# Performance work log

Measured on AMD Instinct MI355X. Metric: run time of the kernel, lower is better.

## Reference

```python
import jax, jax.numpy as jnp
import numpy as np

K, MU, SIGMA = 8, 0.0, 0.1
M, N, D_DIM, T = 512, 1024, 512, 4096


def setup_inputs() -> dict:
    key = jax.random.key(0)
    ks, ke, ka, kd, kl1, kl2 = jax.random.split(key, 6)
    S = jax.random.normal(ks, (N, T), dtype=jnp.float32)
    E = jax.random.normal(ke, (M, T), dtype=jnp.float32)  # raw noise; scaled by sigma/mu in reference
    A = jax.random.uniform(ka, (M, N), dtype=jnp.float32)  # torch.rand init
    Dm = jax.random.normal(kd, (N, D_DIM), dtype=jnp.float32) / jnp.sqrt(N)  # stands in for DCT-transformed randn
    c = jnp.ones((1,), dtype=jnp.float32)
    l1 = 0.1 * jnp.abs(jax.random.normal(kl1, (1,), dtype=jnp.float32)) + 0.05
    l2 = jax.random.normal(kl2, (1,), dtype=jnp.float32)
    # LISTA params per layer; all K layers get the same closed-form init in the original
    U1 = jnp.eye(D_DIM, dtype=jnp.float32) - (1.0 / c[0]) * (Dm.T @ A.T @ A @ Dm)  # [d,d]
    V1 = (1.0 / c[0]) * (Dm.T @ A.T)  # [d,m]
    U = jnp.broadcast_to(U1, (K, D_DIM, D_DIM)).copy()
    V = jnp.broadcast_to(V1, (K, D_DIM, M)).copy()
    H0 = jnp.zeros((D_DIM, T), dtype=jnp.float32)
    return {"S": S, "E": E, "A": A, "D": Dm, "U": U, "V": V, "l1": l1, "l2": l2, "c": c, "H0": H0}


def reference(S, E, A, D, U, V, l1, l2, c, H0):
    # X = A @ S + noise (E ~ randn, scaled as in torch forward)
    X = A @ S + (E * SIGMA + MU)  # [m,T]
    # Self-attention on H0 (the original loop always feeds self.H, the zero buffer,
    # into every layer -- H is never chained). Attention map = softmax((D@H0)^T (D@H0)).
    G = D @ H0                                   # [n,T]
    attn = jax.nn.softmax(G.T @ G, axis=-1)      # [T,T]
    Z = l2[0] * (H0 @ attn)                      # [d,T]
    # All K LISTA updates share the same (H0-derived) Z and X -> batch over layers.
    mat = jnp.einsum('kde,et->kdt', U, Z) + jnp.einsum('kdm,mt->kdt', V, X)  # [K,d,T]
    thres = l1[0] / c[0]
    H_all = jnp.sign(mat) * jnp.maximum(jnp.zeros((), mat.dtype), jnp.abs(mat) - thres)
    H_last = H_all[-1]                           # only the last layer's H survives the loop
    return D @ H_last                            # S_star [n,T]
```

## Files before the change

kernel.cpp:

```cpp
#include <hip/hip_runtime.h>

typedef unsigned short ushort_t;
typedef unsigned int u32;
typedef ushort_t u16x8 __attribute__((ext_vector_type(8)));
typedef ushort_t u16x4 __attribute__((ext_vector_type(4)));
typedef __bf16   bf16x8 __attribute__((ext_vector_type(8)));
typedef float    f32x4  __attribute__((ext_vector_type(4)));

#define T_DIM 4096

__device__ __forceinline__ ushort_t f2bf(float f){
  union { float f; unsigned u; } x; x.f = f;
  unsigned r = x.u + 0x7FFFu + ((x.u >> 16) & 1u);
  return (ushort_t)(r >> 16);
}

__device__ __forceinline__ void gload16(const void* g, void* l){
  __builtin_amdgcn_global_load_lds(
      (const __attribute__((address_space(1))) u32*)g,
      (__attribute__((address_space(3))) u32*)l, 16, 0, 0);
}

__global__ __launch_bounds__(256) void prep_kernel(
    const float* __restrict__ S, const float* __restrict__ A,
    const float* __restrict__ V7, const float* __restrict__ Dm,
    ushort_t* __restrict__ St, ushort_t* __restrict__ Abf,
    ushort_t* __restrict__ Vbf, ushort_t* __restrict__ Dbf)
{
  __shared__ float tile[64][65];
  const int bid = blockIdx.x, tid = threadIdx.x;
  if (bid < 1024){
    const int t0 = (bid & 63) * 64, n0 = (bid >> 6) * 64;
#pragma unroll
    for (int i = 0; i < 4; ++i){
      int g = tid + 256 * i; int row = g >> 4, cq = g & 15;
      const f32x4 v = *(const f32x4*)&S[(size_t)(n0 + row) * T_DIM + t0 + cq * 4];
#pragma unroll
      for (int j = 0; j < 4; ++j) tile[row][cq * 4 + j] = v[j];
    }
    __syncthreads();
#pragma unroll
    for (int i = 0; i < 2; ++i){
      int g = tid + 256 * i; int tl = g >> 3, nq = g & 7;
      u16x8 h;
#pragma unroll
      for (int j = 0; j < 8; ++j) h[j] = f2bf(tile[nq * 8 + j][tl]);
      *(u16x8*)&St[(size_t)(t0 + tl) * 1024 + n0 + ((nq ^ (tl & 7)) << 3)] = h;
    }
  } else {
    int pid = bid - 1024;
    const float* src; ushort_t* dst; int g, ks;
    if (pid < 256)      { src = A;  dst = Abf; g = pid * 256 + tid;        ks = 7; }
    else if (pid < 384) { src = V7; dst = Vbf; g = (pid - 256) * 256 + tid; ks = 6; }
    else                { src = Dm; dst = Dbf; g = (pid - 384) * 256 + tid; ks = 6; }
    const int r = g >> ks, cg = g & ((1 << ks) - 1);
    const int Kd = 8 << ks;
    const size_t base = (size_t)r * Kd + (size_t)cg * 8;
    const f32x4 v0 = *(const f32x4*)&src[base];
    const f32x4 v1 = *(const f32x4*)&src[base + 4];
    u16x8 h;
#pragma unroll
    for (int j = 0; j < 4; ++j){ h[j] = f2bf(v0[j]); h[j + 4] = f2bf(v1[j]); }
    *(u16x8*)&dst[(size_t)r * Kd + ((cg >> 3) << 6) + ((((cg & 7) ^ (r & 7))) << 3)] = h;
  }
}

template<int EPI, int NK>
__global__ __launch_bounds__(512, 2) void gemm_kernel(
    const ushort_t* __restrict__ Ag, const ushort_t* __restrict__ Bg,
    void* __restrict__ Cout, const float* __restrict__ Eptr,
    const float* __restrict__ l1p, const float* __restrict__ cp)
{
  constexpr int KD = NK * 64;
  constexpr bool SWAP = (EPI != 2);
  constexpr int P = SWAP ? 2 : 4;
  constexpr int Q = SWAP ? 4 : 2;
  __shared__ __align__(16) ushort_t As[4][128 * 64];
  __shared__ __align__(16) ushort_t Bs[4][64 * 64];
  __shared__ __align__(16) float Elds[64 * 128];
  const int tid = threadIdx.x;
  const int lane = tid & 63, wid = tid >> 6;
  const int g = wid >> 2;
  const int s = wid & 3;
  const int wm = s >> 1, wn = s & 1;
  const int lr = lane & 15, lq = lane >> 4;
  const int t0 = blockIdx.x * 128, n0 = blockIdx.y * 64;
  const int ltid = tid & 255;

  f32x4 acc[P][Q];
#pragma unroll
  for (int p = 0; p < P; ++p)
#pragma unroll
    for (int q = 0; q < Q; ++q) acc[p][q] = (f32x4){0.f, 0.f, 0.f, 0.f};

  auto stage = [&](int kt){
    const int slot = ((kt & 1) << 1) | ((kt >> 1) & 1);
#pragma unroll
    for (int i = 0; i < 4; ++i){
      int c = i * 256 + ltid;
      gload16(&Ag[(size_t)(t0 + (c >> 3)) * KD + kt * 64 + (c & 7) * 8],
              &As[slot][(i * 256 + (ltid & 192)) * 8]);
    }
#pragma unroll
    for (int i = 0; i < 2; ++i){
      int c = i * 256 + ltid;
      gload16(&Bg[(size_t)(n0 + (c >> 3)) * KD + kt * 64 + (c & 7) * 8],
              &Bs[slot][(i * 256 + (ltid & 192)) * 8]);
    }
  };

  auto compute = [&](int kt){
    const int slot = ((kt & 1) << 1) | ((kt >> 1) & 1);
#pragma unroll
    for (int ksv = 0; ksv < 2; ++ksv){
      const int kb = ksv * 4 + lq;
      bf16x8 a[4], bb[2];
#pragma unroll
      for (int mf = 0; mf < 4; ++mf){
        int r = wm * 64 + mf * 16 + lr;
        a[mf] = *(const bf16x8*)&As[slot][r * 64 + ((kb ^ (r & 7)) << 3)];
      }
#pragma unroll
      for (int nf = 0; nf < 2; ++nf){
        int r = wn * 32 + nf * 16 + lr;
        bb[nf] = *(const bf16x8*)&Bs[slot][r * 64 + ((kb ^ (r & 7)) << 3)];
      }
      __builtin_amdgcn_s_setprio(1);
      if constexpr (SWAP){
#pragma unroll
        for (int nf = 0; nf < 2; ++nf)
#pragma unroll
          for (int mf = 0; mf < 4; ++mf)
            acc[nf][mf] = __builtin_amdgcn_mfma_f32_16x16x32_bf16(
                bb[nf], a[mf], acc[nf][mf], 0, 0, 0);
      } else {
#pragma unroll
        for (int mf = 0; mf < 4; ++mf)
#pragma unroll
          for (int nf = 0; nf < 2; ++nf)
            acc[mf][nf] = __builtin_amdgcn_mfma_f32_16x16x32_bf16(
                a[mf], bb[nf], acc[mf][nf], 0, 0, 0);
      }
      __builtin_amdgcn_s_setprio(0);
    }
  };

  if constexpr (EPI == 0){
#pragma unroll
    for (int i = 0; i < 4; ++i){
      int c = i * 512 + tid;
      gload16(&Eptr[(size_t)(n0 + (c >> 5)) * T_DIM + t0 + (c & 31) * 4],
              (char*)Elds + (size_t)(i * 512 + (tid & 448)) * 16);
    }
    __builtin_amdgcn_sched_barrier(0);
  }
  if (g == 0){ stage(0); stage(2); }
  else       { stage(1); }

  for (int kt = 0; kt < NK; ++kt){
    if ((kt & 1) == g){
      if (kt + 2 < NK) { asm volatile("s_waitcnt vmcnt(6)" ::: "memory"); }
      else             { asm volatile("s_waitcnt vmcnt(0)" ::: "memory"); }
    }
    __builtin_amdgcn_s_barrier();
    __builtin_amdgcn_sched_barrier(0);
    if ((kt & 1) == g){
      compute(kt);
    } else {
      if (kt + 3 < NK) stage(kt + 3);
    }
  }

  float* accs = (float*)&As[0][0];

  if constexpr (SWAP){
    if (g == 1){
#pragma unroll
      for (int nf = 0; nf < 2; ++nf)
#pragma unroll
        for (int mf = 0; mf < 4; ++mf){
          const int tl = wm * 64 + mf * 16 + lr;
          const int em0 = wn * 32 + nf * 16 + lq * 4;
          const int mp = (((em0 >> 3) ^ (tl & 7)) << 3) + (em0 & 7);
          *(f32x4*)&accs[tl * 68 + mp] = acc[nf][mf];
        }
    }
    asm volatile("s_waitcnt lgkmcnt(0)" ::: "memory");
    __builtin_amdgcn_s_barrier();
    if (g == 0){
      const float thres = (EPI == 1) ? (l1p[0] / cp[0]) : 0.f;
#pragma unroll
      for (int nf = 0; nf < 2; ++nf)
#pragma unroll
        for (int mf = 0; mf < 4; ++mf){
          const int tl = wm * 64 + mf * 16 + lr;
          const int em0 = wn * 32 + nf * 16 + lq * 4;
          const int mp = (((em0 >> 3) ^ (tl & 7)) << 3) + (em0 & 7);
          f32x4 v = *(const f32x4*)&accs[tl * 68 + mp];
          v += acc[nf][mf];
          if constexpr (EPI == 0){
#pragma unroll
            for (int j = 0; j < 4; ++j)
              v[j] += 0.1f * Elds[(em0 + j) * 128 + tl];
          } else {
#pragma unroll
            for (int j = 0; j < 4; ++j){
              float av = fabsf(v[j]) - thres;
              v[j] = av > 0.f ? (v[j] > 0.f ? av : -av) : 0.f;
            }
          }
          *(f32x4*)&accs[tl * 68 + mp] = v;
        }
    }
    asm volatile("s_waitcnt lgkmcnt(0)" ::: "memory");
    __builtin_amdgcn_s_barrier();
    ushort_t* OT = (ushort_t*)Cout;
#pragma unroll
    for (int i = 0; i < 2; ++i){
      const int c = i * 512 + tid;
      const int t = c >> 3, mb = (c & 7) * 8;
      const f32x4 a0 = *(const f32x4*)&accs[t * 68 + mb];
      const f32x4 a1 = *(const f32x4*)&accs[t * 68 + mb + 4];
      u16x8 h;
#pragma unroll
      for (int j = 0; j < 4; ++j){ h[j] = f2bf(a0[j]); h[j + 4] = f2bf(a1[j]); }
      *(u16x8*)&OT[(size_t)(t0 + t) * 512 + n0 + mb] = h;
    }
  } else {
    if (g == 1){
#pragma unroll
      for (int mf = 0; mf < 4; ++mf)
#pragma unroll
        for (int nf = 0; nf < 2; ++nf){
          const int tl0 = wm * 64 + mf * 16 + lq * 4;
          const int nl  = wn * 32 + nf * 16 + lr;
          *(f32x4*)&accs[nl * 132 + tl0] = acc[mf][nf];
        }
    }
    asm volatile("s_waitcnt lgkmcnt(0)" ::: "memory");
    __builtin_amdgcn_s_barrier();
    if (g == 0){
#pragma unroll
      for (int mf = 0; mf < 4; ++mf)
#pragma unroll
        for (int nf = 0; nf < 2; ++nf){
          const int tl0 = wm * 64 + mf * 16 + lq * 4;
          const int nl  = wn * 32 + nf * 16 + lr;
          f32x4 v = *(const f32x4*)&accs[nl * 132 + tl0];
          v += acc[mf][nf];
          *(f32x4*)&accs[nl * 132 + tl0] = v;
        }
    }
    asm volatile("s_waitcnt lgkmcnt(0)" ::: "memory");
    __builtin_amdgcn_s_barrier();
    float* O = (float*)Cout;
#pragma unroll
    for (int i = 0; i < 4; ++i){
      const int c = i * 512 + tid;
      const int n = c >> 5, t4 = (c & 31) * 4;
      *(f32x4*)&O[(size_t)(n0 + n) * T_DIM + t0 + t4] =
          *(const f32x4*)&accs[n * 132 + t4];
    }
  }
}

extern "C" void kernel_launch(void* const* d_in, const int* in_sizes, int n_in,
                              void* d_out, int out_size, void* d_ws, size_t ws_size,
                              hipStream_t stream)
{
  const float* S  = (const float*)d_in[0];
  const float* E  = (const float*)d_in[1];
  const float* A  = (const float*)d_in[2];
  const float* Dm = (const float*)d_in[3];
  const float* V  = (const float*)d_in[5];
  const float* l1 = (const float*)d_in[6];
  const float* c  = (const float*)d_in[8];

  char* ws = (char*)d_ws;
  ushort_t* St  = (ushort_t*)(ws);
  ushort_t* XT  = (ushort_t*)(ws + (size_t)( 8u << 20));
  ushort_t* HT  = (ushort_t*)(ws + (size_t)(12u << 20));
  ushort_t* Abf = (ushort_t*)(ws + (size_t)(16u << 20));
  ushort_t* Vbf = (ushort_t*)(ws + (size_t)(17u << 20));
  ushort_t* Dbf = (ushort_t*)(ws + (size_t)(17u << 20) + (512u << 10));
  const float* V7 = V + (size_t)7 * 512 * 512;

  prep_kernel<<<1664, 256, 0, stream>>>(S, A, V7, Dm, St, Abf, Vbf, Dbf);
  gemm_kernel<0, 16><<<dim3(32, 8), 512, 0, stream>>>(St, Abf, (void*)XT, E, nullptr, nullptr);
  gemm_kernel<1, 8><<<dim3(32, 8), 512, 0, stream>>>(XT, Vbf, (void*)HT, nullptr, l1, c);
  gemm_kernel<2, 8><<<dim3(32, 16), 512, 0, stream>>>(HT, Dbf, d_out, nullptr, nullptr, nullptr);
}
```

Measured before the change: 39.66 us.

## Fuse S transpose and bf16 conversion into first GEMM's load pipeline

Removes the separate S transpose/convert pass from the prep kernel. The first GEMM now loads fp32 S tiles into registers, converts them to bf16 and writes them transposed into LDS inside its double-buffered pipeline. This eliminates writing and re-reading the 8 MB bf16 St intermediate and shrinks the prep kernel. In exchange, each n-block re-reads S in fp32, which doubles the re-read bytes, and the extra staging registers add pressure.

```diff
diff --git a/kernel.cpp b/kernel.cpp
--- a/kernel.cpp
+++ b/kernel.cpp
@@ -22,54 +22,206 @@
 }
 
 __global__ __launch_bounds__(256) void prep_kernel(
-    const float* __restrict__ S, const float* __restrict__ A,
-    const float* __restrict__ V7, const float* __restrict__ Dm,
-    ushort_t* __restrict__ St, ushort_t* __restrict__ Abf,
+    const float* __restrict__ A, const float* __restrict__ V7,
+    const float* __restrict__ Dm, ushort_t* __restrict__ Abf,
     ushort_t* __restrict__ Vbf, ushort_t* __restrict__ Dbf)
 {
-  __shared__ float tile[64][65];
-  const int bid = blockIdx.x, tid = threadIdx.x;
-  if (bid < 1024){
-    const int t0 = (bid & 63) * 64, n0 = (bid >> 6) * 64;
-#pragma unroll
-    for (int i = 0; i < 4; ++i){
-      int g = tid + 256 * i; int row = g >> 4, cq = g & 15;
-      const f32x4 v = *(const f32x4*)&S[(size_t)(n0 + row) * T_DIM + t0 + cq * 4];
-#pragma unroll
-      for (int j = 0; j < 4; ++j) tile[row][cq * 4 + j] = v[j];
-    }
-    __syncthreads();
+  const int pid = blockIdx.x, tid = threadIdx.x;
+  const float* src; ushort_t* dst; int g, ks;
+  if (pid < 256)      { src = A;  dst = Abf; g = pid * 256 + tid;        ks = 7; }
+  else if (pid < 384) { src = V7; dst = Vbf; g = (pid - 256) * 256 + tid; ks = 6; }
+  else                { src = Dm; dst = Dbf; g = (pid - 384) * 256 + tid; ks = 6; }
+  const int r = g >> ks, cg = g & ((1 << ks) - 1);
+  const int Kd = 8 << ks;
+  const size_t base = (size_t)r * Kd + (size_t)cg * 8;
+  const f32x4 v0 = *(const f32x4*)&src[base];
+  const f32x4 v1 = *(const f32x4*)&src[base + 4];
+  u16x8 h;
+#pragma unroll
+  for (int j = 0; j < 4; ++j){ h[j] = f2bf(v0[j]); h[j + 4] = f2bf(v1[j]); }
+  *(u16x8*)&dst[(size_t)r * Kd + ((cg >> 3) << 6) + ((((cg & 7) ^ (r & 7))) << 3)] = h;
+}
+
+#define ISSUE_S(kt, rS) do {                                                   \
+  _Pragma("unroll") for (int i_ = 0; i_ < 2; ++i_){                            \
+    const int task_ = i_ * 256 + ltid;                                         \
+    const int rg_ = task_ >> 5, tq_ = task_ & 31;                              \
+    _Pragma("unroll") for (int ii_ = 0; ii_ < 4; ++ii_)                        \
+      rS[i_ * 4 + ii_] = *(const f32x4*)&S[                                    \
+          (size_t)((kt) * 64 + rg_ * 4 + ii_) * T_DIM + t0 + tq_ * 4];         \
+  } } while (0)
+
+#define WRITE_S(kt, rS) do {                                                   \
+  const int slot_ = (((kt) & 1) << 1) | (((kt) >> 1) & 1);                     \
+  _Pragma("unroll") for (int i_ = 0; i_ < 2; ++i_){                            \
+    const int task_ = i_ * 256 + ltid;                                         \
+    const int rg_ = task_ >> 5, tq_ = task_ & 31;                              \
+    _Pragma("unroll") for (int j_ = 0; j_ < 4; ++j_){                          \
+      const int t_ = tq_ * 4 + j_;                                             \
+      u16x4 w_;                                                                \
+      _Pragma("unroll") for (int ii_ = 0; ii_ < 4; ++ii_)                      \
+        w_[ii_] = f2bf(rS[i_ * 4 + ii_][j_]);                                  \
+      *(u16x4*)&As[slot_][t_ * 64 + (((rg_ >> 1) ^ (t_ & 7)) << 3)             \
+                          + ((rg_ & 1) << 2)] = w_;                            \
+    }                                                                          \
+  } } while (0)
+
+#define G1_STEP(kt, RLD, RWR) do {                                             \
+  if (((kt) & 1) == g){                                                        \
+    __builtin_amdgcn_s_barrier();                                              \
+    __builtin_amdgcn_sched_barrier(0);                                         \
+    compute(kt);                                                               \
+  } else {                                                                     \
+    if ((kt) + 3 < NK) ISSUE_S((kt) + 3, RLD);                                 \
+    __builtin_amdgcn_s_barrier();                                              \
+    if ((kt) + 3 < NK){                                                        \
+      issueB((kt) + 3);                                                        \
+      asm volatile("s_waitcnt vmcnt(10)" ::: "memory");                        \
+    } else {                                                                   \
+      asm volatile("s_waitcnt vmcnt(0)" ::: "memory");                         \
+    }                                                                          \
+    __builtin_amdgcn_sched_barrier(0);                                         \
+    if ((kt) + 1 < NK) WRITE_S((kt) + 1, RWR);                                 \
+    asm volatile("s_waitcnt lgkmcnt(0)" ::: "memory");                         \
+  } } while (0)
+
+__global__ __launch_bounds__(512, 2) void gemm1_kernel(
+    const float* __restrict__ S, const ushort_t* __restrict__ Bg,
+    const float* __restrict__ Eptr, ushort_t* __restrict__ XT)
+{
+  constexpr int NK = 16;
+  __shared__ __align__(16) ushort_t As[4][128 * 64];
+  __shared__ __align__(16) ushort_t Bs[4][64 * 64];
+  __shared__ __align__(16) float Elds[64 * 128];
+  const int tid = threadIdx.x;
+  const int lane = tid & 63, wid = tid >> 6;
+  const int g = wid >> 2, s = wid & 3;
+  const int wm = s >> 1, wn = s & 1;
+  const int lr = lane & 15, lq = lane >> 4;
+  const int t0 = blockIdx.x * 128, n0 = blockIdx.y * 64;
+  const int ltid = tid & 255;
+
+  f32x4 acc[2][4];
+#pragma unroll
+  for (int p = 0; p < 2; ++p)
+#pragma unroll
+    for (int q = 0; q < 4; ++q) acc[p][q] = (f32x4){0.f, 0.f, 0.f, 0.f};
+
+  f32x4 rSa[8], rSb[8];
+
+  auto issueB = [&](int kt){
+    const int slot = ((kt & 1) << 1) | ((kt >> 1) & 1);
 #pragma unroll
     for (int i = 0; i < 2; ++i){
-      int g = tid + 256 * i; int tl = g >> 3, nq = g & 7;
-      u16x8 h;
-#pragma unroll
-      for (int j = 0; j < 8; ++j) h[j] = f2bf(tile[nq * 8 + j][tl]);
-      *(u16x8*)&St[(size_t)(t0 + tl) * 1024 + n0 + ((nq ^ (tl & 7)) << 3)] = h;
-    }
+      int c = i * 256 + ltid;
+      gload16(&Bg[(size_t)(n0 + (c >> 3)) * 1024 + kt * 64 + (c & 7) * 8],
+              &Bs[slot][(i * 256 + (ltid & 192)) * 8]);
+    }
+  };
+
+  auto compute = [&](int kt){
+    const int slot = ((kt & 1) << 1) | ((kt >> 1) & 1);
+#pragma unroll
+    for (int ksv = 0; ksv < 2; ++ksv){
+      const int kb = ksv * 4 + lq;
+      bf16x8 a[4], bb[2];
+#pragma unroll
+      for (int mf = 0; mf < 4; ++mf){
+        int r = wm * 64 + mf * 16 + lr;
+        a[mf] = *(const bf16x8*)&As[slot][r * 64 + ((kb ^ (r & 7)) << 3)];
+      }
+#pragma unroll
+      for (int nf = 0; nf < 2; ++nf){
+        int r = wn * 32 + nf * 16 + lr;
+        bb[nf] = *(const bf16x8*)&Bs[slot][r * 64 + ((kb ^ (r & 7)) << 3)];
+      }
+      __builtin_amdgcn_s_setprio(1);
+#pragma unroll
+      for (int nf = 0; nf < 2; ++nf)
+#pragma unroll
+        for (int mf = 0; mf < 4; ++mf)
+          acc[nf][mf] = __builtin_amdgcn_mfma_f32_16x16x32_bf16(
+              bb[nf], a[mf], acc[nf][mf], 0, 0, 0);
+      __builtin_amdgcn_s_setprio(0);
+    }
+  };
+
+#pragma unroll
+  for (int i = 0; i < 4; ++i){
+    int c = i * 512 + tid;
+    gload16(&Eptr[(size_t)(n0 + (c >> 5)) * T_DIM + t0 + (c & 31) * 4],
+            (char*)Elds + (size_t)(i * 512 + (tid & 448)) * 16);
+  }
+  __builtin_amdgcn_sched_barrier(0);
+  if (g == 0){
+    ISSUE_S(0, rSa); issueB(0);
+    asm volatile("s_waitcnt vmcnt(0)" ::: "memory");
+    WRITE_S(0, rSa);
+    ISSUE_S(2, rSb); issueB(2);
   } else {
-    int pid = bid - 1024;
-    const float* src; ushort_t* dst; int g, ks;
-    if (pid < 256)      { src = A;  dst = Abf; g = pid * 256 + tid;        ks = 7; }
-    else if (pid < 384) { src = V7; dst = Vbf; g = (pid - 256) * 256 + tid; ks = 6; }
-    else                { src = Dm; dst = Dbf; g = (pid - 384) * 256 + tid; ks = 6; }
-    const int r = g >> ks, cg = g & ((1 << ks) - 1);
-    const int Kd = 8 << ks;
-    const size_t base = (size_t)r * Kd + (size_t)cg * 8;
-    const f32x4 v0 = *(const f32x4*)&src[base];
-    const f32x4 v1 = *(const f32x4*)&src[base + 4];
+    ISSUE_S(1, rSb); issueB(1);
+  }
+  asm volatile("s_waitcnt lgkmcnt(0)" ::: "memory");
+
+#pragma unroll 1
+  for (int kt0 = 0; kt0 < NK; kt0 += 4){
+    G1_STEP(kt0 + 0, rSa, rSb);
+    G1_STEP(kt0 + 1, rSa, rSb);
+    G1_STEP(kt0 + 2, rSb, rSa);
+    G1_STEP(kt0 + 3, rSb, rSa);
+  }
+  asm volatile("s_waitcnt vmcnt(0)" ::: "memory");
+
+  float* accs = (float*)&As[0][0];
+  if (g == 1){
+#pragma unroll
+    for (int nf = 0; nf < 2; ++nf)
+#pragma unroll
+      for (int mf = 0; mf < 4; ++mf){
+        const int tl = wm * 64 + mf * 16 + lr;
+        const int em0 = wn * 32 + nf * 16 + lq * 4;
+        const int mp = (((em0 >> 3) ^ (tl & 7)) << 3) + (em0 & 7);
+        *(f32x4*)&accs[tl * 68 + mp] = acc[nf][mf];
+      }
+  }
+  asm volatile("s_waitcnt lgkmcnt(0)" ::: "memory");
+  __builtin_amdgcn_s_barrier();
+  if (g == 0){
+#pragma unroll
+    for (int nf = 0; nf < 2; ++nf)
+#pragma unroll
+      for (int mf = 0; mf < 4; ++mf){
+        const int tl = wm * 64 + mf * 16 + lr;
+        const int em0 = wn * 32 + nf * 16 + lq * 4;
+        const int mp = (((em0 >> 3) ^ (tl & 7)) << 3) + (em0 & 7);
+        f32x4 v = *(const f32x4*)&accs[tl * 68 + mp];
+        v += acc[nf][mf];
+#pragma unroll
+        for (int j = 0; j < 4; ++j)
+          v[j] += 0.1f * Elds[(em0 + j) * 128 + tl];
+        *(f32x4*)&accs[tl * 68 + mp] = v;
+      }
+  }
+  asm volatile("s_waitcnt lgkmcnt(0)" ::: "memory");
+  __builtin_amdgcn_s_barrier();
+#pragma unroll
+  for (int i = 0; i < 2; ++i){
+    const int c = i * 512 + tid;
+    const int t = c >> 3, mb = (c & 7) * 8;
+    const f32x4 a0 = *(const f32x4*)&accs[t * 68 + mb];
+    const f32x4 a1 = *(const f32x4*)&accs[t * 68 + mb + 4];
     u16x8 h;
 #pragma unroll
-    for (int j = 0; j < 4; ++j){ h[j] = f2bf(v0[j]); h[j + 4] = f2bf(v1[j]); }
-    *(u16x8*)&dst[(size_t)r * Kd + ((cg >> 3) << 6) + ((((cg & 7) ^ (r & 7))) << 3)] = h;
+    for (int j = 0; j < 4; ++j){ h[j] = f2bf(a0[j]); h[j + 4] = f2bf(a1[j]); }
+    *(u16x8*)&XT[(size_t)(t0 + t) * 512 + n0 + mb] = h;
   }
 }
 
 template<int EPI, int NK>
 __global__ __launch_bounds__(512, 2) void gemm_kernel(
     const ushort_t* __restrict__ Ag, const ushort_t* __restrict__ Bg,
-    void* __restrict__ Cout, const float* __restrict__ Eptr,
-    const float* __restrict__ l1p, const float* __restrict__ cp)
+    void* __restrict__ Cout, const float* __restrict__ l1p,
+    const float* __restrict__ cp)
 {
   constexpr int KD = NK * 64;
   constexpr bool SWAP = (EPI != 2);
@@ -77,7 +229,6 @@
   constexpr int Q = SWAP ? 4 : 2;
   __shared__ __align__(16) ushort_t As[4][128 * 64];
   __shared__ __align__(16) ushort_t Bs[4][64 * 64];
-  __shared__ __align__(16) float Elds[64 * 128];
   const int tid = threadIdx.x;
   const int lane = tid & 63, wid = tid >> 6;
   const int g = wid >> 2;
@@ -145,15 +296,6 @@
     }
   };
 
-  if constexpr (EPI == 0){
-#pragma unroll
-    for (int i = 0; i < 4; ++i){
-      int c = i * 512 + tid;
-      gload16(&Eptr[(size_t)(n0 + (c >> 5)) * T_DIM + t0 + (c & 31) * 4],
-              (char*)Elds + (size_t)(i * 512 + (tid & 448)) * 16);
-    }
-    __builtin_amdgcn_sched_barrier(0);
-  }
   if (g == 0){ stage(0); stage(2); }
   else       { stage(1); }
 
@@ -172,7 +314,6 @@
   }
 
   float* accs = (float*)&As[0][0];
-
   if constexpr (SWAP){
     if (g == 1){
 #pragma unroll
@@ -188,7 +329,7 @@
     asm volatile("s_waitcnt lgkmcnt(0)" ::: "memory");
     __builtin_amdgcn_s_barrier();
     if (g == 0){
-      const float thres = (EPI == 1) ? (l1p[0] / cp[0]) : 0.f;
+      const float thres = l1p[0] / cp[0];
 #pragma unroll
       for (int nf = 0; nf < 2; ++nf)
 #pragma unroll
@@ -198,16 +339,10 @@
           const int mp = (((em0 >> 3) ^ (tl & 7)) << 3) + (em0 & 7);
           f32x4 v = *(const f32x4*)&accs[tl * 68 + mp];
           v += acc[nf][mf];
-          if constexpr (EPI == 0){
-#pragma unroll
-            for (int j = 0; j < 4; ++j)
-              v[j] += 0.1f * Elds[(em0 + j) * 128 + tl];
-          } else {
-#pragma unroll
-            for (int j = 0; j < 4; ++j){
-              float av = fabsf(v[j]) - thres;
-              v[j] = av > 0.f ? (v[j] > 0.f ? av : -av) : 0.f;
-            }
+#pragma unroll
+          for (int j = 0; j < 4; ++j){
+            float av = fabsf(v[j]) - thres;
+            v[j] = av > 0.f ? (v[j] > 0.f ? av : -av) : 0.f;
           }
           *(f32x4*)&accs[tl * 68 + mp] = v;
         }
@@ -277,16 +412,15 @@
   const float* c  = (const float*)d_in[8];
 
   char* ws = (char*)d_ws;
-  ushort_t* St  = (ushort_t*)(ws);
-  ushort_t* XT  = (ushort_t*)(ws + (size_t)( 8u << 20));
-  ushort_t* HT  = (ushort_t*)(ws + (size_t)(12u << 20));
-  ushort_t* Abf = (ushort_t*)(ws + (size_t)(16u << 20));
-  ushort_t* Vbf = (ushort_t*)(ws + (size_t)(17u << 20));
-  ushort_t* Dbf = (ushort_t*)(ws + (size_t)(17u << 20) + (512u << 10));
+  ushort_t* XT  = (ushort_t*)(ws);
+  ushort_t* HT  = (ushort_t*)(ws + (size_t)( 4u << 20));
+  ushort_t* Abf = (ushort_t*)(ws + (size_t)( 8u << 20));
+  ushort_t* Vbf = (ushort_t*)(ws + (size_t)( 9u << 20));
+  ushort_t* Dbf = (ushort_t*)(ws + (size_t)(10u << 20));
   const float* V7 = V + (size_t)7 * 512 * 512;
 
-  prep_kernel<<<1664, 256, 0, stream>>>(S, A, V7, Dm, St, Abf, Vbf, Dbf);
-  gemm_kernel<0, 16><<<dim3(32, 8), 512, 0, stream>>>(St, Abf, (void*)XT, E, nullptr, nullptr);
-  gemm_kernel<1, 8><<<dim3(32, 8), 512, 0, stream>>>(XT, Vbf, (void*)HT, nullptr, l1, c);
-  gemm_kernel<2, 8><<<dim3(32, 16), 512, 0, stream>>>(HT, Dbf, d_out, nullptr, nullptr, nullptr);
-}
+  prep_kernel<<<640, 256, 0, stream>>>(A, V7, Dm, Abf, Vbf, Dbf);
+  gemm1_kernel<<<dim3(32, 8), 512, 0, stream>>>(S, Abf, E, XT);
+  gemm_kernel<1, 8><<<dim3(32, 8), 512, 0, stream>>>(XT, Vbf, (void*)HT, l1, c);
+  gemm_kernel<2, 8><<<dim3(32, 16), 512, 0, stream>>>(HT, Dbf, d_out, nullptr, nullptr);
+}
```

After: 46.19 us. +16.5%, slower.
